# Optimization experiments

Hardware: AMD Instinct MI355X
Metric: run time of the kernel (lower is better)

The kernel has to match this reference:

```python
import jax, jax.numpy as jnp
import numpy as np

B, T, D = 4096, 200, 64
H1, H2 = 80, 40
C = 64  # cate_count


def setup_inputs() -> dict:
    key = jax.random.key(0)
    ks = jax.random.split(key, 12)
    q = jax.random.normal(ks[0], (B, D), dtype=jnp.float32)
    k = jax.random.normal(ks[1], (B, T, D), dtype=jnp.float32)
    mask = jax.random.randint(ks[2], (B, T), 0, 2, dtype=jnp.int32)
    hist_cate = jax.random.randint(ks[3], (B, T), 0, C, dtype=jnp.int32)
    # attention MLP params (Dense(80, PReLU), Dense(40, PReLU), Dense(1))
    W1 = jax.random.normal(ks[4], (4 * D, H1), dtype=jnp.float32) * (1.0 / np.sqrt(4 * D))
    b1 = jnp.zeros((H1,), dtype=jnp.float32)
    a1 = jnp.full((H1,), 0.25, dtype=jnp.float32)  # PReLU slopes
    W2 = jax.random.normal(ks[5], (H1, H2), dtype=jnp.float32) * (1.0 / np.sqrt(H1))
    b2 = jnp.zeros((H2,), dtype=jnp.float32)
    a2 = jnp.full((H2,), 0.25, dtype=jnp.float32)
    Wf = jax.random.normal(ks[6], (H2, 1), dtype=jnp.float32) * (1.0 / np.sqrt(H2))
    bf = jnp.zeros((1,), dtype=jnp.float32)
    return {
        "q": q, "k": k, "mask": mask, "hist_cate": hist_cate,
        "cate_count": C,
        "W1": W1, "b1": b1, "a1": a1,
        "W2": W2, "b2": b2, "a2": a2,
        "Wf": Wf, "bf": bf,
    }


def _prelu(x, alpha):
    return jnp.maximum(x, 0.0) + alpha * jnp.minimum(x, 0.0)


def reference(q, k, mask, hist_cate, cate_count, W1, b1, a1, W2, b2, a2, Wf, bf):
    b, t, d = k.shape
    qe = jnp.broadcast_to(q[:, None, :], (b, t, d))          # tile q over seq
    info = jnp.concatenate([qe, k, qe - k, qe * k], axis=-1)  # [B,T,4D]
    h = _prelu(info @ W1 + b1, a1)                            # [B,T,H1]
    h = _prelu(h @ W2 + b2, a2)                               # [B,T,H2]
    logits = (h @ Wf + bf)[..., 0]                            # [B,T]
    neg = jnp.float32(-2 ** 32 + 1)
    logits = jnp.where(mask == 0, neg, logits)
    logits = logits / jnp.sqrt(jnp.float32(d))
    w = jax.nn.softmax(logits, axis=-1)                       # [B,T]
    user_interest = jnp.einsum('bt,btd->bd', w, k)            # [B,D]
    # fused per-category masked weighted pooling (replaces Python loop)
    onehot = (hist_cate[:, None, :] == jnp.arange(cate_count, dtype=hist_cate.dtype)[None, :, None])  # [B,C,T]
    wc = w[:, None, :] * onehot.astype(w.dtype)               # [B,C,T]
    wc = wc / (jnp.sum(wc, axis=-1, keepdims=True) + 1e-10)
    cate_hidden = jnp.einsum('bct,btd->bcd', wc, k)           # [B,C,D]
    return user_interest, cate_hidden
```

## Files before the change

### kernel.cpp

```cpp
#include <hip/hip_runtime.h>

typedef unsigned short u16;
typedef short short8 __attribute__((ext_vector_type(8)));
typedef float f32x4 __attribute__((ext_vector_type(4)));

#define NEG_MASK -4294967295.0f

__device__ __forceinline__ u16 f2bf(float f) {
    unsigned int x = __float_as_uint(f);
    unsigned int r = (x + 0x7FFFu + ((x >> 16) & 1u)) >> 16;
    return (u16)r;
}
__device__ __forceinline__ short8 cvt8(float4 a, float4 b) {
    union { short8 v; u16 u[8]; } r;
    r.u[0] = f2bf(a.x); r.u[1] = f2bf(a.y); r.u[2] = f2bf(a.z); r.u[3] = f2bf(a.w);
    r.u[4] = f2bf(b.x); r.u[5] = f2bf(b.y); r.u[6] = f2bf(b.z); r.u[7] = f2bf(b.w);
    return r.v;
}

__global__ __launch_bounds__(256) void din_kernel(
    const float* __restrict__ qp, const float* __restrict__ kp,
    const int* __restrict__ maskp, const int* __restrict__ catep,
    const float* __restrict__ W1p, const float* __restrict__ b1p,
    const float* __restrict__ a1p, const float* __restrict__ W2p,
    const float* __restrict__ b2p, const float* __restrict__ a2p,
    const float* __restrict__ wfp, const float* __restrict__ bfp,
    float* __restrict__ outp)
{
    __shared__ __align__(16) u16 MtW2t[80*72 + 48*104];
    __shared__ __align__(16) float logits_s[200];
    __shared__ __align__(16) float q_s[64], qW_s[80], a1_s[80];
    __shared__ __align__(16) float a2_s[48], b2_s[48], wf_s[48];
    __shared__ float s_c[64], red_s[8], bf_s;
    __shared__ int cate_s[200];
    __shared__ int mask_s[200];

    u16* Mt  = MtW2t;
    u16* W2t = MtW2t + 80*72;
    float* cate_acc = (float*)MtW2t;
    float* qW2 = logits_s;

    const int tid  = threadIdx.x;
    const int b    = blockIdx.x;
    const int wid  = tid >> 6;
    const int lane = tid & 63;
    const int i16  = lane & 15;
    const int q4   = lane >> 4;
    const float* kb = kp + (size_t)b * 12800;

    {
        unsigned int* w2z = (unsigned int*)W2t;
        for (int i = tid; i < (48*104)/2; i += 256) w2z[i] = 0u;
    }
    if (tid < 64) { s_c[tid] = 0.f; q_s[tid] = qp[(size_t)b*64 + tid]; }
    if (tid < 48) {
        wf_s[tid] = (tid < 40) ? wfp[tid] : 0.f;
        a2_s[tid] = (tid < 40) ? a2p[tid] : 0.f;
        b2_s[tid] = (tid < 40) ? b2p[tid] : 0.f;
    }
    if (tid < 80) a1_s[tid] = a1p[tid];
    if (tid == 0) bf_s = bfp[0];
    if (tid < 200) {
        cate_s[tid] = catep[(size_t)b*200 + tid];
        mask_s[tid] = maskp[(size_t)b*200 + tid];
    }
    __syncthreads();

    #pragma unroll 4
    for (int j = tid; j < 5120; j += 256) {
        int d = j / 80, h = j - d*80;
        float m = W1p[5120 + j] - W1p[10240 + j] + q_s[d] * W1p[15360 + j];
        Mt[h*72 + d] = f2bf(m);
    }
    if (tid < 160) {
        int p = tid / 80, h = tid - p*80;
        float acc0 = 0.f, acc1 = 0.f;
        int d0 = p * 32;
        #pragma unroll 4
        for (int d = d0; d < d0 + 32; d += 2) {
            acc0 += q_s[d]   * (W1p[d*80 + h]     + W1p[(128+d)*80 + h]);
            acc1 += q_s[d+1] * (W1p[(d+1)*80 + h] + W1p[(129+d)*80 + h]);
        }
        qW2[tid] = acc0 + acc1;
    }
    #pragma unroll 4
    for (int e = tid; e < 3200; e += 256) {
        int n = e % 40, kk = e / 40;
        W2t[n*104 + kk] = f2bf(W2p[e]);
    }
    __syncthreads();
    if (tid < 80) qW_s[tid] = b1p[tid] + qW2[tid] + qW2[80 + tid];
    __syncthreads();

    {
        int mt = wid;
        float4 f0, f1, f2, f3;
        {
            int arow = mt*16 + i16; if (arow > 199) arow = 199;
            const float4* kr = (const float4*)(kb + arow*64);
            f0 = kr[2*q4];     f1 = kr[2*q4 + 1];
            f2 = kr[8 + 2*q4]; f3 = kr[9 + 2*q4];
        }
        const int srcA = i16 + ((lane & 16) << 1);
        const int srcB = srcA + 16;
        const bool hi4 = (q4 >> 1) != 0;
        for (; mt < 13; mt += 4) {
            short8 ka0 = cvt8(f0, f1);
            short8 ka1 = cvt8(f2, f3);
            {
                int nmt = mt + 4; if (nmt > 12) nmt = 12;
                int narow = nmt*16 + i16; if (narow > 199) narow = 199;
                const float4* nkr = (const float4*)(kb + narow*64);
                f0 = nkr[2*q4];     f1 = nkr[2*q4 + 1];
                f2 = nkr[8 + 2*q4]; f3 = nkr[9 + 2*q4];
            }
            unsigned int P0[2], P1[2], P2[2], P3[2], P4[2];
#define G1(nt, Pd) { \
            const int n0 = (nt)*16; \
            float4 qw4 = *(const float4*)&qW_s[n0 + q4*4]; \
            f32x4 acc = { qw4.x, qw4.y, qw4.z, qw4.w }; \
            short8 m0 = *(const short8*)&Mt[(n0+i16)*72 + q4*8]; \
            short8 m1 = *(const short8*)&Mt[(n0+i16)*72 + 32 + q4*8]; \
            acc = __builtin_amdgcn_mfma_f32_16x16x32_bf16(m0, ka0, acc, 0, 0, 0); \
            acc = __builtin_amdgcn_mfma_f32_16x16x32_bf16(m1, ka1, acc, 0, 0, 0); \
            float4 al4 = *(const float4*)&a1_s[n0 + q4*4]; \
            float y0 = (acc[0] > 0.f) ? acc[0] : al4.x * acc[0]; \
            float y1 = (acc[1] > 0.f) ? acc[1] : al4.y * acc[1]; \
            float y2 = (acc[2] > 0.f) ? acc[2] : al4.z * acc[2]; \
            float y3 = (acc[3] > 0.f) ? acc[3] : al4.w * acc[3]; \
            Pd[0] = (unsigned int)f2bf(y0) | ((unsigned int)f2bf(y1) << 16); \
            Pd[1] = (unsigned int)f2bf(y2) | ((unsigned int)f2bf(y3) << 16); }
            G1(0, P0) G1(1, P1) G1(2, P2) G1(3, P3) G1(4, P4)
#undef G1
            union BW { unsigned int w[4]; short8 v; } B0, B1, B2;
            {
                int xa, xb, ya, yb, za, zb, wa, wb;
                xa = __shfl((int)P0[0], srcA); xb = __shfl((int)P0[1], srcA);
                ya = __shfl((int)P0[0], srcB); yb = __shfl((int)P0[1], srcB);
                za = __shfl((int)P1[0], srcA); zb = __shfl((int)P1[1], srcA);
                wa = __shfl((int)P1[0], srcB); wb = __shfl((int)P1[1], srcB);
                B0.w[0] = hi4 ? (unsigned)za : (unsigned)xa;
                B0.w[1] = hi4 ? (unsigned)zb : (unsigned)xb;
                B0.w[2] = hi4 ? (unsigned)wa : (unsigned)ya;
                B0.w[3] = hi4 ? (unsigned)wb : (unsigned)yb;
                xa = __shfl((int)P2[0], srcA); xb = __shfl((int)P2[1], srcA);
                ya = __shfl((int)P2[0], srcB); yb = __shfl((int)P2[1], srcB);
                za = __shfl((int)P3[0], srcA); zb = __shfl((int)P3[1], srcA);
                wa = __shfl((int)P3[0], srcB); wb = __shfl((int)P3[1], srcB);
                B1.w[0] = hi4 ? (unsigned)za : (unsigned)xa;
                B1.w[1] = hi4 ? (unsigned)zb : (unsigned)xb;
                B1.w[2] = hi4 ? (unsigned)wa : (unsigned)ya;
                B1.w[3] = hi4 ? (unsigned)wb : (unsigned)yb;
                xa = __shfl((int)P4[0], srcA); xb = __shfl((int)P4[1], srcA);
                ya = __shfl((int)P4[0], srcB); yb = __shfl((int)P4[1], srcB);
                B2.w[0] = hi4 ? 0u : (unsigned)xa;
                B2.w[1] = hi4 ? 0u : (unsigned)xb;
                B2.w[2] = hi4 ? 0u : (unsigned)ya;
                B2.w[3] = hi4 ? 0u : (unsigned)yb;
            }
            float part = 0.f;
            #pragma unroll
            for (int gt = 0; gt < 3; ++gt) {
                const int g0 = gt*16;
                float4 b24 = *(const float4*)&b2_s[g0 + q4*4];
                f32x4 acc = { b24.x, b24.y, b24.z, b24.w };
                short8 w0 = *(const short8*)&W2t[(g0+i16)*104 + q4*8];
                short8 w1 = *(const short8*)&W2t[(g0+i16)*104 + 32 + q4*8];
                short8 w2 = *(const short8*)&W2t[(g0+i16)*104 + 64 + q4*8];
                acc = __builtin_amdgcn_mfma_f32_16x16x32_bf16(w0, B0.v, acc, 0, 0, 0);
                acc = __builtin_amdgcn_mfma_f32_16x16x32_bf16(w1, B1.v, acc, 0, 0, 0);
                acc = __builtin_amdgcn_mfma_f32_16x16x32_bf16(w2, B2.v, acc, 0, 0, 0);
                float4 a24 = *(const float4*)&a2_s[g0 + q4*4];
                float4 wf4 = *(const float4*)&wf_s[g0 + q4*4];
                part += ((acc[0] > 0.f) ? acc[0] : a24.x * acc[0]) * wf4.x;
                part += ((acc[1] > 0.f) ? acc[1] : a24.y * acc[1]) * wf4.y;
                part += ((acc[2] > 0.f) ? acc[2] : a24.z * acc[2]) * wf4.z;
                part += ((acc[3] > 0.f) ? acc[3] : a24.w * acc[3]) * wf4.w;
            }
            part += __shfl_xor(part, 16, 64);
            part += __shfl_xor(part, 32, 64);
            if (lane < 16) {
                int t = mt*16 + lane;
                if (t < 200) {
                    float v = (mask_s[t] == 0) ? NEG_MASK : (bf_s + part);
                    logits_s[t] = v * 0.125f;
                }
            }
        }
    }
    __syncthreads();

    {
        float4 z = {0.f, 0.f, 0.f, 0.f};
        float4* ca4 = (float4*)cate_acc;
        for (int i = tid; i < 1024; i += 256) ca4[i] = z;
    }
    const int t0 = wid * 50;
    float kd[10];
    #pragma unroll
    for (int j = 0; j < 10; ++j) kd[j] = kb[(t0 + j)*64 + lane];

    float x = (tid < 200) ? logits_s[tid] : -3.0e38f;
    float m = x;
    #pragma unroll
    for (int off = 32; off >= 1; off >>= 1) m = fmaxf(m, __shfl_xor(m, off, 64));
    if (lane == 0) red_s[wid] = m;
    __syncthreads();
    float mx = fmaxf(fmaxf(red_s[0], red_s[1]), fmaxf(red_s[2], red_s[3]));
    float e = (tid < 200) ? __expf(x - mx) : 0.f;
    float s = e;
    #pragma unroll
    for (int off = 32; off >= 1; off >>= 1) s += __shfl_xor(s, off, 64);
    if (lane == 0) red_s[4 + wid] = s;
    __syncthreads();
    float tot = red_s[4] + red_s[5] + red_s[6] + red_s[7];
    float wv = e / tot;
    if (tid < 200) {
        logits_s[tid] = wv;
        if (wv > 0.f) atomicAdd(&s_c[cate_s[tid]], wv);
    }
    __syncthreads();

    for (int i = 0; i < 50; i += 10) {
        float nkd[10];
        const bool more = (i + 10 < 50);
        if (more) {
            #pragma unroll
            for (int j = 0; j < 10; ++j) nkd[j] = kb[(t0 + i + 10 + j)*64 + lane];
        }
        #pragma unroll
        for (int j = 0; j < 10; ++j) {
            float w = logits_s[t0 + i + j];
            if (w > 0.f) atomicAdd(&cate_acc[cate_s[t0 + i + j]*64 + lane], w * kd[j]);
        }
        if (more) {
            #pragma unroll
            for (int j = 0; j < 10; ++j) kd[j] = nkd[j];
        }
    }
    __syncthreads();

    if (tid < 64) {
        float ui = 0.f;
        #pragma unroll 8
        for (int c = 0; c < 64; ++c) ui += cate_acc[c*64 + tid];
        outp[(size_t)b*64 + tid] = ui;
    }
    {
        float* outc = outp + (size_t)(4096*64) + (size_t)b*4096;
        #pragma unroll
        for (int ii = 0; ii < 4; ++ii) {
            int i = tid*4 + ii*1024;
            float inv = 1.0f / (s_c[i >> 6] + 1e-10f);
            float4 v = *(const float4*)&cate_acc[i];
            v.x *= inv; v.y *= inv; v.z *= inv; v.w *= inv;
            *(float4*)&outc[i] = v;
        }
    }
}

extern "C" void kernel_launch(void* const* d_in, const int* in_sizes, int n_in,
                              void* d_out, int out_size, void* d_ws, size_t ws_size,
                              hipStream_t stream) {
    din_kernel<<<4096, 256, 0, stream>>>(
        (const float*)d_in[0],
        (const float*)d_in[1],
        (const int*)d_in[2],
        (const int*)d_in[3],
        (const float*)d_in[5],
        (const float*)d_in[6],
        (const float*)d_in[7],
        (const float*)d_in[8],
        (const float*)d_in[9],
        (const float*)d_in[10],
        (const float*)d_in[11],
        (const float*)d_in[12],
        (float*)d_out);
}
```

Measured before the change: 487.1 us.

## Split fused DIN kernel into separate MLP-logit and softmax-pooling kernels

The single fused kernel becomes two launches. The first computes the attention MLP logits and writes them to a workspace buffer. The second reloads the logits, does the softmax and the per-category pooling with its own LDS allocation and a launch bound of 8 blocks per CU. The aim is to give each phase a lighter register and LDS footprint so more waves stay resident. The cost is an extra launch, a global round trip for the logits, and a second read of k that may no longer hit in cache.

```diff
diff --git a/kernel.cpp b/kernel.cpp
--- a/kernel.cpp
+++ b/kernel.cpp
@@ -18,27 +18,23 @@
     return r.v;
 }
 
-__global__ __launch_bounds__(256) void din_kernel(
+__global__ __launch_bounds__(256) void din_mlp(
     const float* __restrict__ qp, const float* __restrict__ kp,
-    const int* __restrict__ maskp, const int* __restrict__ catep,
+    const int* __restrict__ maskp,
     const float* __restrict__ W1p, const float* __restrict__ b1p,
     const float* __restrict__ a1p, const float* __restrict__ W2p,
     const float* __restrict__ b2p, const float* __restrict__ a2p,
     const float* __restrict__ wfp, const float* __restrict__ bfp,
-    float* __restrict__ outp)
+    float* __restrict__ wsf)
 {
     __shared__ __align__(16) u16 MtW2t[80*72 + 48*104];
-    __shared__ __align__(16) float logits_s[200];
     __shared__ __align__(16) float q_s[64], qW_s[80], a1_s[80];
     __shared__ __align__(16) float a2_s[48], b2_s[48], wf_s[48];
-    __shared__ float s_c[64], red_s[8], bf_s;
-    __shared__ int cate_s[200];
+    __shared__ float qW2[160], bf_s;
     __shared__ int mask_s[200];
 
     u16* Mt  = MtW2t;
     u16* W2t = MtW2t + 80*72;
-    float* cate_acc = (float*)MtW2t;
-    float* qW2 = logits_s;
 
     const int tid  = threadIdx.x;
     const int b    = blockIdx.x;
@@ -52,7 +48,7 @@
         unsigned int* w2z = (unsigned int*)W2t;
         for (int i = tid; i < (48*104)/2; i += 256) w2z[i] = 0u;
     }
-    if (tid < 64) { s_c[tid] = 0.f; q_s[tid] = qp[(size_t)b*64 + tid]; }
+    if (tid < 64) q_s[tid] = qp[(size_t)b*64 + tid];
     if (tid < 48) {
         wf_s[tid] = (tid < 40) ? wfp[tid] : 0.f;
         a2_s[tid] = (tid < 40) ? a2p[tid] : 0.f;
@@ -60,10 +56,7 @@
     }
     if (tid < 80) a1_s[tid] = a1p[tid];
     if (tid == 0) bf_s = bfp[0];
-    if (tid < 200) {
-        cate_s[tid] = catep[(size_t)b*200 + tid];
-        mask_s[tid] = maskp[(size_t)b*200 + tid];
-    }
+    if (tid < 200) mask_s[tid] = maskp[(size_t)b*200 + tid];
     __syncthreads();
 
     #pragma unroll 4
@@ -96,7 +89,7 @@
         int mt = wid;
         float4 f0, f1, f2, f3;
         {
-            int arow = mt*16 + i16; if (arow > 199) arow = 199;
+            int arow = mt*16 + i16;
             const float4* kr = (const float4*)(kb + arow*64);
             f0 = kr[2*q4];     f1 = kr[2*q4 + 1];
             f2 = kr[8 + 2*q4]; f3 = kr[9 + 2*q4];
@@ -183,24 +176,42 @@
                 int t = mt*16 + lane;
                 if (t < 200) {
                     float v = (mask_s[t] == 0) ? NEG_MASK : (bf_s + part);
-                    logits_s[t] = v * 0.125f;
+                    wsf[(size_t)b*200 + t] = v * 0.125f;
                 }
             }
         }
     }
-    __syncthreads();
-
+}
+
+__global__ __launch_bounds__(256, 8) void din_pool(
+    const float* __restrict__ kp, const int* __restrict__ catep,
+    const float* __restrict__ wsf, float* __restrict__ outp)
+{
+    __shared__ __align__(16) float cate_acc[4096];
+    __shared__ float logits_s[200];
+    __shared__ float s_c[64], red_s[8];
+    __shared__ int cate_s[200];
+
+    const int tid  = threadIdx.x;
+    const int b    = blockIdx.x;
+    const int wid  = tid >> 6;
+    const int lane = tid & 63;
+    const float* kb = kp + (size_t)b * 12800;
+
+    if (tid < 64) s_c[tid] = 0.f;
+    if (tid < 200) cate_s[tid] = catep[(size_t)b*200 + tid];
     {
         float4 z = {0.f, 0.f, 0.f, 0.f};
         float4* ca4 = (float4*)cate_acc;
-        for (int i = tid; i < 1024; i += 256) ca4[i] = z;
+        #pragma unroll
+        for (int i = 0; i < 4; ++i) ca4[tid + i*256] = z;
     }
     const int t0 = wid * 50;
     float kd[10];
     #pragma unroll
     for (int j = 0; j < 10; ++j) kd[j] = kb[(t0 + j)*64 + lane];
 
-    float x = (tid < 200) ? logits_s[tid] : -3.0e38f;
+    float x = (tid < 200) ? wsf[(size_t)b*200 + tid] : -3.0e38f;
     float m = x;
     #pragma unroll
     for (int off = 32; off >= 1; off >>= 1) m = fmaxf(m, __shfl_xor(m, off, 64));
@@ -262,11 +273,11 @@
 extern "C" void kernel_launch(void* const* d_in, const int* in_sizes, int n_in,
                               void* d_out, int out_size, void* d_ws, size_t ws_size,
                               hipStream_t stream) {
-    din_kernel<<<4096, 256, 0, stream>>>(
+    float* wsf = (float*)d_ws;
+    din_mlp<<<4096, 256, 0, stream>>>(
         (const float*)d_in[0],
         (const float*)d_in[1],
         (const int*)d_in[2],
-        (const int*)d_in[3],
         (const float*)d_in[5],
         (const float*)d_in[6],
         (const float*)d_in[7],
@@ -275,5 +286,10 @@
         (const float*)d_in[10],
         (const float*)d_in[11],
         (const float*)d_in[12],
+        wsf);
+    din_pool<<<4096, 256, 0, stream>>>(
+        (const float*)d_in[1],
+        (const int*)d_in[3],
+        wsf,
         (float*)d_out);
 }
```

Result: slower. 520.0 us (+6.8%).
